# Performance work log

Hardware: AMD Instinct MI355X
Metric: run time of the kernel (lower is better)

## Reference

```python
import jax, jax.numpy as jnp
import numpy as np

B, T, C = 16, 4096, 64  # batch, seq_len, n_embd == head_size


def setup_inputs() -> dict:
    key = jax.random.key(0)
    k1, k2, k3, k4 = jax.random.split(key, 4)
    x = jax.random.normal(k1, (B, T, C), dtype=jnp.float32)
    Wq = jax.random.normal(k2, (C, C), dtype=jnp.float32) * (C ** -0.5)
    Wk = jax.random.normal(k3, (C, C), dtype=jnp.float32) * (C ** -0.5)
    Wv = jax.random.normal(k4, (C, C), dtype=jnp.float32) * (C ** -0.5)
    return {"x": x, "Wq": Wq, "Wk": Wk, "Wv": Wv}


def reference(x, Wq, Wk, Wv):
    # Single-head causal self-attention (dropout rate = 0.0 in source -> identity).
    q = jnp.einsum('btc,cd->btd', x, Wq)  # [B,T,D]
    k = jnp.einsum('btc,cd->btd', x, Wk)  # [B,T,D]
    v = jnp.einsum('btc,cd->btd', x, Wv)  # [B,T,D]
    scale = q.shape[-1] ** -0.5
    wei = jnp.einsum('btd,bsd->bts', q, k) * scale  # [B,T,T] scores
    causal = jnp.tril(jnp.ones((T, T), dtype=bool))  # [T,T]
    wei = jnp.where(causal[None, :, :], wei, jnp.finfo(wei.dtype).min)
    wei = jax.nn.softmax(wei, axis=-1)
    out = jnp.einsum('bts,bsd->btd', wei, v)  # [B,T,D]
    return out
```

## Files before the change

kernel.cpp:

```cpp
#include <hip/hip_runtime.h>
#include <hip/hip_bf16.h>
#include <math.h>

#define BATCH 16
#define SEQ 4096
#define HDIM 64

typedef __attribute__((ext_vector_type(8))) short bf16x8;
typedef __attribute__((ext_vector_type(4))) float f32x4;
typedef __attribute__((ext_vector_type(8))) unsigned short us8;

#define QSCALE 0.1803368801111601f

static __device__ __forceinline__ float exp2_fast(float x) {
#if __has_builtin(__builtin_amdgcn_exp2f)
    return __builtin_amdgcn_exp2f(x);
#else
    float r; asm("v_exp_f32 %0, %1" : "=v"(r) : "v"(x)); return r;
#endif
}

static __device__ __forceinline__ void load_lds16(const void* g, void* l) {
    __builtin_amdgcn_global_load_lds(
        (const __attribute__((address_space(1))) unsigned int*)g,
        (__attribute__((address_space(3))) unsigned int*)l,
        16, 0, 0);
}

static __device__ __forceinline__ unsigned short bf16bits(float f) {
    __hip_bfloat16 h = __float2bfloat16(f);
    return *(unsigned short*)&h;
}

__global__ __launch_bounds__(256)
void qkv_mfma_kernel(const float* __restrict__ x,
                     const float* __restrict__ Wq,
                     const float* __restrict__ Wk,
                     const float* __restrict__ Wv,
                     __hip_bfloat16* __restrict__ qb,
                     __hip_bfloat16* __restrict__ kb,
                     __hip_bfloat16* __restrict__ vt) {
    __shared__ __attribute__((aligned(16))) __hip_bfloat16 swt[3 * 64 * 64];
    __shared__ __attribute__((aligned(16))) __hip_bfloat16 sout[64][80];
    const int tid = threadIdx.x;
    const int wv = tid >> 6;
    const int lane = tid & 63;
    const int quad = lane >> 4;
    const int ml = lane & 15;
    const size_t row0 = (size_t)blockIdx.x * 64;
    const int batch = (int)(row0 >> 12);
    const int t0 = (int)(row0 & 4095);

    #pragma unroll
    for (int mat = 0; mat < 3; ++mat) {
        const float* W = (mat == 0) ? Wq : (mat == 1) ? Wk : Wv;
        const float sc = (mat == 0) ? QSCALE : 1.0f;
        const int n = tid & 63;
        #pragma unroll
        for (int i = 0; i < 16; ++i) {
            const int f = i * 256 + tid;
            const int k = f >> 6;
            swt[mat * 4096 + n * 64 + (((k >> 3) ^ (n & 7)) << 3) + (k & 7)] =
                __float2bfloat16(W[f] * sc);
        }
    }

    bf16x8 a0, a1;
    {
        const float4* xr = (const float4*)(x + (row0 + wv * 16 + ml) * HDIM);
        float4 lo = xr[quad * 2], hi = xr[quad * 2 + 1];
        float t8[8] = {lo.x, lo.y, lo.z, lo.w, hi.x, hi.y, hi.z, hi.w};
        #pragma unroll
        for (int j = 0; j < 8; ++j) a0[j] = (short)bf16bits(t8[j]);
        lo = xr[8 + quad * 2]; hi = xr[9 + quad * 2];
        float u8[8] = {lo.x, lo.y, lo.z, lo.w, hi.x, hi.y, hi.z, hi.w};
        #pragma unroll
        for (int j = 0; j < 8; ++j) a1[j] = (short)bf16bits(u8[j]);
    }
    __syncthreads();

    #pragma unroll
    for (int mat = 0; mat < 3; ++mat) {
        const __hip_bfloat16* wb = swt + mat * 4096;
        f32x4 acc[4];
        #pragma unroll
        for (int nt = 0; nt < 4; ++nt) {
            const int n = nt * 16 + ml;
            const int nx = n & 7;
            const bf16x8 bl = *(const bf16x8*)(wb + (size_t)n * 64 + (size_t)((quad) ^ nx) * 8);
            const bf16x8 bh = *(const bf16x8*)(wb + (size_t)n * 64 + (size_t)((quad + 4) ^ nx) * 8);
            acc[nt] = __builtin_amdgcn_mfma_f32_16x16x32_bf16(a0, bl, (f32x4){0.f,0.f,0.f,0.f}, 0, 0, 0);
            acc[nt] = __builtin_amdgcn_mfma_f32_16x16x32_bf16(a1, bh, acc[nt], 0, 0, 0);
        }

        if (mat < 2) {
            #pragma unroll
            for (int nt = 0; nt < 4; ++nt)
                #pragma unroll
                for (int r = 0; r < 4; ++r)
                    sout[wv * 16 + quad * 4 + r][nt * 16 + ml] = __float2bfloat16(acc[nt][r]);
        } else {
            #pragma unroll
            for (int nt = 0; nt < 4; ++nt)
                #pragma unroll
                for (int r = 0; r < 4; ++r)
                    sout[nt * 16 + ml][(wv >> 1) * 32 + quad * 8 + (wv & 1) * 4 + r] =
                        __float2bfloat16(acc[nt][r]);
        }
        __syncthreads();
        __hip_bfloat16* dst = (mat == 0) ? qb : (mat == 1) ? kb : vt;
        #pragma unroll
        for (int c2 = 0; c2 < 2; ++c2) {
            const int cc = c2 * 256 + tid;
            const int row = cc >> 3, g = cc & 7;
            us8 u = *(const us8*)&sout[row][g * 8];
            if (mat < 2)
                *(us8*)(dst + (row0 + row) * HDIM + g * 8) = u;
            else
                *(us8*)(dst + ((size_t)batch * HDIM + row) * SEQ + t0 + g * 8) = u;
        }
        __syncthreads();
    }
}

__global__ __launch_bounds__(256, 4)
void flash_mfma_kernel(const __hip_bfloat16* __restrict__ qb,
                       const __hip_bfloat16* __restrict__ kbuf,
                       const __hip_bfloat16* __restrict__ vt,
                       float* __restrict__ out) {
    __shared__ __attribute__((aligned(16))) __hip_bfloat16 sk[64 * 64];
    __shared__ __attribute__((aligned(16))) __hip_bfloat16 sv[64 * 64];
    __shared__ __attribute__((aligned(16))) float smerge[2][64][18];
    const int tid = threadIdx.x;
    const int wv = tid >> 6;
    const int lane = tid & 63;
    const int quad = lane >> 4;
    const int ml = lane & 15;
    const int mh = wv & 1;
    const int kh = wv >> 1;

    const int id = blockIdx.x;
    const int b = id & 15;
    const int t = id >> 4;
    const int hi2 = t >> 4, mid = t & 15;
    const int qt = (hi2 == 0) ? (63 - mid)
                 : (hi2 == 1) ? (32 + mid)
                 : (hi2 == 2) ? (31 - mid) : mid;
    const int qbw = qt * 64 + mh * 32;
    const size_t bb = (size_t)b * SEQ * HDIM;

    const __hip_bfloat16* Q = qb + bb;
    const __hip_bfloat16* K = kbuf + bb;
    const __hip_bfloat16* VT = vt + bb;

    bf16x8 bq[2][2];
    #pragma unroll
    for (int qi = 0; qi < 2; ++qi)
        #pragma unroll
        for (int h = 0; h < 2; ++h)
            bq[qi][h] = *(const bf16x8*)(Q + (size_t)(qbw + qi * 16 + ml) * HDIM + h * 32 + quad * 8);

    bf16x8 ones8;
    #pragma unroll
    for (int j = 0; j < 8; ++j) ones8[j] = (short)0x3F80;

    f32x4 acc[4][2];
    #pragma unroll
    for (int nt = 0; nt < 4; ++nt)
        #pragma unroll
        for (int qi = 0; qi < 2; ++qi) acc[nt][qi] = (f32x4){0.f, 0.f, 0.f, 0.f};
    f32x4 lacc[2] = {(f32x4){0.f,0.f,0.f,0.f}, (f32x4){0.f,0.f,0.f,0.f}};

    const int s0 = wv * 128 + lane;
    const int s1 = s0 + 64;
    const int r0row = s0 >> 3, r0ch = (s0 & 7) ^ (r0row & 7);
    const int r1row = s1 >> 3, r1ch = (s1 & 7) ^ (r1row & 7);
    __hip_bfloat16* ldsb0k = sk + (size_t)(wv * 128) * 8;
    __hip_bfloat16* ldsb1k = sk + (size_t)(wv * 128 + 64) * 8;
    __hip_bfloat16* ldsb0v = sv + (size_t)(wv * 128) * 8;
    __hip_bfloat16* ldsb1v = sv + (size_t)(wv * 128 + 64) * 8;

    const int rx = ml & 7;
    const int ntiles = qt + 1;
    for (int tile = 0; tile < ntiles; ++tile) {
        const int kb0 = tile * 64;
        __syncthreads();
        load_lds16(K + (size_t)(kb0 + r0row) * HDIM + r0ch * 8, ldsb0k);
        load_lds16(K + (size_t)(kb0 + r1row) * HDIM + r1ch * 8, ldsb1k);
        load_lds16(VT + (size_t)r0row * SEQ + kb0 + r0ch * 8, ldsb0v);
        load_lds16(VT + (size_t)r1row * SEQ + kb0 + r1ch * 8, ldsb1v);
        asm volatile("s_waitcnt vmcnt(0)" ::: "memory");
        __syncthreads();

        if (tile == qt && kh == 1 && mh == 0) continue;

        f32x4 st[2][2];
        #pragma unroll
        for (int kt = 0; kt < 2; ++kt) {
            const int row = kh * 32 + kt * 16 + ml;
            const int rb = row << 3, rxx = row & 7;
            const bf16x8 kl = *(const bf16x8*)(sk + (size_t)((rb | (quad ^ rxx)) * 8));
            const bf16x8 khi = *(const bf16x8*)(sk + (size_t)((rb | ((quad + 4) ^ rxx)) * 8));
            #pragma unroll
            for (int qi = 0; qi < 2; ++qi) {
                st[kt][qi] = __builtin_amdgcn_mfma_f32_16x16x32_bf16(kl, bq[qi][0], (f32x4){0.f,0.f,0.f,0.f}, 0, 0, 0);
                st[kt][qi] = __builtin_amdgcn_mfma_f32_16x16x32_bf16(khi, bq[qi][1], st[kt][qi], 0, 0, 0);
            }
        }

        const bool edge = (tile == qt);
        bf16x8 p8[2];
        #pragma unroll
        for (int qi = 0; qi < 2; ++qi) {
            const int q = qbw + qi * 16 + ml;
            #pragma unroll
            for (int half = 0; half < 2; ++half)
                #pragma unroll
                for (int r = 0; r < 4; ++r) {
                    const int key = kb0 + kh * 32 + half * 16 + quad * 4 + r;
                    float pv = exp2_fast(st[half][qi][r]);
                    if (edge && (key > q)) pv = 0.f;
                    p8[qi][half * 4 + r] = (short)bf16bits(pv);
                }
        }

        lacc[0] = __builtin_amdgcn_mfma_f32_16x16x32_bf16(ones8, p8[0], lacc[0], 0, 0, 0);
        lacc[1] = __builtin_amdgcn_mfma_f32_16x16x32_bf16(ones8, p8[1], lacc[1], 0, 0, 0);
        #pragma unroll
        for (int nt = 0; nt < 4; ++nt) {
            const int row = nt * 16 + ml;
            const int rb = row << 3, rxx = row & 7;
            const bf16x8 va = *(const bf16x8*)(sv + (size_t)((rb | ((kh * 4 + quad) ^ rxx)) * 8));
            acc[nt][0] = __builtin_amdgcn_mfma_f32_16x16x32_bf16(va, p8[0], acc[nt][0], 0, 0, 0);
            acc[nt][1] = __builtin_amdgcn_mfma_f32_16x16x32_bf16(va, p8[1], acc[nt][1], 0, 0, 0);
        }
    }

    #pragma unroll
    for (int qi = 0; qi < 2; ++qi) {
        __syncthreads();
        if (kh == 1) {
            float* mrow = smerge[mh][lane];
            #pragma unroll
            for (int nt = 0; nt < 4; ++nt)
                #pragma unroll
                for (int r = 0; r < 4; ++r) mrow[nt * 4 + r] = acc[nt][qi][r];
            mrow[16] = lacc[qi][0];
        }
        __syncthreads();
        if (kh == 0) {
            const float* mrow = smerge[mh][lane];
            const float inv = 1.0f / (lacc[qi][0] + mrow[16]);
            float* orow = out + bb + (size_t)(qbw + qi * 16 + ml) * HDIM;
            #pragma unroll
            for (int nt = 0; nt < 4; ++nt) {
                float4 o;
                o.x = (acc[nt][qi][0] + mrow[nt * 4 + 0]) * inv;
                o.y = (acc[nt][qi][1] + mrow[nt * 4 + 1]) * inv;
                o.z = (acc[nt][qi][2] + mrow[nt * 4 + 2]) * inv;
                o.w = (acc[nt][qi][3] + mrow[nt * 4 + 3]) * inv;
                *(float4*)(orow + nt * 16 + quad * 4) = o;
            }
        }
    }
}

extern "C" void kernel_launch(void* const* d_in, const int* in_sizes, int n_in,
                              void* d_out, int out_size, void* d_ws, size_t ws_size,
                              hipStream_t stream) {
    const float* x  = (const float*)d_in[0];
    const float* Wq = (const float*)d_in[1];
    const float* Wk = (const float*)d_in[2];
    const float* Wv = (const float*)d_in[3];
    float* outp = (float*)d_out;

    const size_t elems = (size_t)BATCH * SEQ * HDIM;
    __hip_bfloat16* qb = (__hip_bfloat16*)d_ws;
    __hip_bfloat16* kb = qb + elems;
    __hip_bfloat16* vt = kb + elems;

    qkv_mfma_kernel<<<dim3(BATCH * SEQ / 64), 256, 0, stream>>>(x, Wq, Wk, Wv, qb, kb, vt);
    flash_mfma_kernel<<<dim3(BATCH * SEQ / 64), 256, 0, stream>>>(qb, kb, vt, outp);
}
```

Measured before the change: 129.7 us.

## Load K/V fragments directly from global into registers, drop LDS staging

Each wave now reads its K and V^T MFMA fragments straight from global memory into registers, where before the whole block staged them through LDS with global_load_lds and two barriers per tile. K fragments for the next tile are prefetched while the current tile computes, and the wave that would skip the last causal tile now shortens its loop instead. This removes the per-tile __syncthreads and the LDS traffic. In exchange, K/V data is fetched redundantly by the waves that share it (more L2/global requests), the V loads are not prefetched, and register pressure rises.

```diff
diff --git a/kernel.cpp b/kernel.cpp
--- a/kernel.cpp
+++ b/kernel.cpp
@@ -18,13 +18,6 @@
 #else
     float r; asm("v_exp_f32 %0, %1" : "=v"(r) : "v"(x)); return r;
 #endif
-}
-
-static __device__ __forceinline__ void load_lds16(const void* g, void* l) {
-    __builtin_amdgcn_global_load_lds(
-        (const __attribute__((address_space(1))) unsigned int*)g,
-        (__attribute__((address_space(3))) unsigned int*)l,
-        16, 0, 0);
 }
 
 static __device__ __forceinline__ unsigned short bf16bits(float f) {
@@ -128,8 +121,6 @@
                        const __hip_bfloat16* __restrict__ kbuf,
                        const __hip_bfloat16* __restrict__ vt,
                        float* __restrict__ out) {
-    __shared__ __attribute__((aligned(16))) __hip_bfloat16 sk[64 * 64];
-    __shared__ __attribute__((aligned(16))) __hip_bfloat16 sv[64 * 64];
     __shared__ __attribute__((aligned(16))) float smerge[2][64][18];
     const int tid = threadIdx.x;
     const int wv = tid >> 6;
@@ -171,41 +162,41 @@
         for (int qi = 0; qi < 2; ++qi) acc[nt][qi] = (f32x4){0.f, 0.f, 0.f, 0.f};
     f32x4 lacc[2] = {(f32x4){0.f,0.f,0.f,0.f}, (f32x4){0.f,0.f,0.f,0.f}};
 
-    const int s0 = wv * 128 + lane;
-    const int s1 = s0 + 64;
-    const int r0row = s0 >> 3, r0ch = (s0 & 7) ^ (r0row & 7);
-    const int r1row = s1 >> 3, r1ch = (s1 & 7) ^ (r1row & 7);
-    __hip_bfloat16* ldsb0k = sk + (size_t)(wv * 128) * 8;
-    __hip_bfloat16* ldsb1k = sk + (size_t)(wv * 128 + 64) * 8;
-    __hip_bfloat16* ldsb0v = sv + (size_t)(wv * 128) * 8;
-    __hip_bfloat16* ldsb1v = sv + (size_t)(wv * 128 + 64) * 8;
-
-    const int rx = ml & 7;
-    const int ntiles = qt + 1;
+    const __hip_bfloat16* kp = K + (size_t)(kh * 32 + ml) * HDIM + quad * 8;
+    const __hip_bfloat16* vp = VT + (size_t)ml * SEQ + (kh * 4 + quad) * 8;
+
+    const int ntiles = qt + 1 - ((mh == 0 && kh == 1) ? 1 : 0);
+
+    bf16x8 kcur[2][2], knext[2][2], vf[4];
+    #pragma unroll
+    for (int kt = 0; kt < 2; ++kt)
+        #pragma unroll
+        for (int h = 0; h < 2; ++h)
+            kcur[kt][h] = *(const bf16x8*)(kp + kt * 16 * HDIM + h * 32);
+
     for (int tile = 0; tile < ntiles; ++tile) {
         const int kb0 = tile * 64;
-        __syncthreads();
-        load_lds16(K + (size_t)(kb0 + r0row) * HDIM + r0ch * 8, ldsb0k);
-        load_lds16(K + (size_t)(kb0 + r1row) * HDIM + r1ch * 8, ldsb1k);
-        load_lds16(VT + (size_t)r0row * SEQ + kb0 + r0ch * 8, ldsb0v);
-        load_lds16(VT + (size_t)r1row * SEQ + kb0 + r1ch * 8, ldsb1v);
-        asm volatile("s_waitcnt vmcnt(0)" ::: "memory");
-        __syncthreads();
-
-        if (tile == qt && kh == 1 && mh == 0) continue;
+
+        #pragma unroll
+        for (int nt = 0; nt < 4; ++nt)
+            vf[nt] = *(const bf16x8*)(vp + (size_t)nt * 16 * SEQ + kb0);
 
         f32x4 st[2][2];
         #pragma unroll
-        for (int kt = 0; kt < 2; ++kt) {
-            const int row = kh * 32 + kt * 16 + ml;
-            const int rb = row << 3, rxx = row & 7;
-            const bf16x8 kl = *(const bf16x8*)(sk + (size_t)((rb | (quad ^ rxx)) * 8));
-            const bf16x8 khi = *(const bf16x8*)(sk + (size_t)((rb | ((quad + 4) ^ rxx)) * 8));
+        for (int kt = 0; kt < 2; ++kt)
             #pragma unroll
             for (int qi = 0; qi < 2; ++qi) {
-                st[kt][qi] = __builtin_amdgcn_mfma_f32_16x16x32_bf16(kl, bq[qi][0], (f32x4){0.f,0.f,0.f,0.f}, 0, 0, 0);
-                st[kt][qi] = __builtin_amdgcn_mfma_f32_16x16x32_bf16(khi, bq[qi][1], st[kt][qi], 0, 0, 0);
+                st[kt][qi] = __builtin_amdgcn_mfma_f32_16x16x32_bf16(kcur[kt][0], bq[qi][0], (f32x4){0.f,0.f,0.f,0.f}, 0, 0, 0);
+                st[kt][qi] = __builtin_amdgcn_mfma_f32_16x16x32_bf16(kcur[kt][1], bq[qi][1], st[kt][qi], 0, 0, 0);
             }
+
+        if (tile + 1 < ntiles) {
+            const __hip_bfloat16* kn = kp + (size_t)(tile + 1) * 64 * HDIM;
+            #pragma unroll
+            for (int kt = 0; kt < 2; ++kt)
+                #pragma unroll
+                for (int h = 0; h < 2; ++h)
+                    knext[kt][h] = *(const bf16x8*)(kn + kt * 16 * HDIM + h * 32);
         }
 
         const bool edge = (tile == qt);
@@ -228,12 +219,15 @@
         lacc[1] = __builtin_amdgcn_mfma_f32_16x16x32_bf16(ones8, p8[1], lacc[1], 0, 0, 0);
         #pragma unroll
         for (int nt = 0; nt < 4; ++nt) {
-            const int row = nt * 16 + ml;
-            const int rb = row << 3, rxx = row & 7;
-            const bf16x8 va = *(const bf16x8*)(sv + (size_t)((rb | ((kh * 4 + quad) ^ rxx)) * 8));
-            acc[nt][0] = __builtin_amdgcn_mfma_f32_16x16x32_bf16(va, p8[0], acc[nt][0], 0, 0, 0);
-            acc[nt][1] = __builtin_amdgcn_mfma_f32_16x16x32_bf16(va, p8[1], acc[nt][1], 0, 0, 0);
-        }
+            acc[nt][0] = __builtin_amdgcn_mfma_f32_16x16x32_bf16(vf[nt], p8[0], acc[nt][0], 0, 0, 0);
+            acc[nt][1] = __builtin_amdgcn_mfma_f32_16x16x32_bf16(vf[nt], p8[1], acc[nt][1], 0, 0, 0);
+        }
+
+        #pragma unroll
+        for (int kt = 0; kt < 2; ++kt)
+            #pragma unroll
+            for (int h = 0; h < 2; ++h)
+                kcur[kt][h] = knext[kt][h];
     }
 
     #pragma unroll
```

Result: slower. 196.5 us (+51.6%).

## Double-buffer K/V tiles in LDS to overlap loads with MFMA compute

Applied to the files above, without the earlier changes.

Replaces the single K and V LDS buffers with one 32KB shared array that holds two K/V tile slots. The next tile is prefetched through global_load_lds into the alternate slot while the current tile is computed, so each iteration needs one barrier instead of two. The merge scratch space is aliased onto the same array after the loop. LDS use per block doubles, which may reduce how many blocks fit per CU, though it likely stays within the launch-bounds target of 4.

```diff
diff --git a/kernel.cpp b/kernel.cpp
--- a/kernel.cpp
+++ b/kernel.cpp
@@ -128,9 +128,8 @@
                        const __hip_bfloat16* __restrict__ kbuf,
                        const __hip_bfloat16* __restrict__ vt,
                        float* __restrict__ out) {
-    __shared__ __attribute__((aligned(16))) __hip_bfloat16 sk[64 * 64];
-    __shared__ __attribute__((aligned(16))) __hip_bfloat16 sv[64 * 64];
-    __shared__ __attribute__((aligned(16))) float smerge[2][64][18];
+    __shared__ __attribute__((aligned(16))) __hip_bfloat16 smem[16384];
+
     const int tid = threadIdx.x;
     const int wv = tid >> 6;
     const int lane = tid & 63;
@@ -175,67 +174,81 @@
     const int s1 = s0 + 64;
     const int r0row = s0 >> 3, r0ch = (s0 & 7) ^ (r0row & 7);
     const int r1row = s1 >> 3, r1ch = (s1 & 7) ^ (r1row & 7);
-    __hip_bfloat16* ldsb0k = sk + (size_t)(wv * 128) * 8;
-    __hip_bfloat16* ldsb1k = sk + (size_t)(wv * 128 + 64) * 8;
-    __hip_bfloat16* ldsb0v = sv + (size_t)(wv * 128) * 8;
-    __hip_bfloat16* ldsb1v = sv + (size_t)(wv * 128 + 64) * 8;
-
-    const int rx = ml & 7;
+    const int d0 = (wv * 128) * 8;
+    const int d1 = (wv * 128 + 64) * 8;
+
     const int ntiles = qt + 1;
+
+    load_lds16(K + (size_t)r0row * HDIM + r0ch * 8, smem + d0);
+    load_lds16(K + (size_t)r1row * HDIM + r1ch * 8, smem + d1);
+    load_lds16(VT + (size_t)r0row * SEQ + r0ch * 8, smem + 8192 + d0);
+    load_lds16(VT + (size_t)r1row * SEQ + r1ch * 8, smem + 8192 + d1);
+    asm volatile("s_waitcnt vmcnt(0)" ::: "memory");
+    __syncthreads();
+
     for (int tile = 0; tile < ntiles; ++tile) {
         const int kb0 = tile * 64;
-        __syncthreads();
-        load_lds16(K + (size_t)(kb0 + r0row) * HDIM + r0ch * 8, ldsb0k);
-        load_lds16(K + (size_t)(kb0 + r1row) * HDIM + r1ch * 8, ldsb1k);
-        load_lds16(VT + (size_t)r0row * SEQ + kb0 + r0ch * 8, ldsb0v);
-        load_lds16(VT + (size_t)r1row * SEQ + kb0 + r1ch * 8, ldsb1v);
+        const int sel = (tile & 1) * 4096;
+        const int nsel = 4096 - sel;
+        const __hip_bfloat16* sk = smem + sel;
+        const __hip_bfloat16* sv = smem + 8192 + sel;
+
+        if (tile + 1 < ntiles) {
+            const int nk = kb0 + 64;
+            load_lds16(K + (size_t)(nk + r0row) * HDIM + r0ch * 8, smem + nsel + d0);
+            load_lds16(K + (size_t)(nk + r1row) * HDIM + r1ch * 8, smem + nsel + d1);
+            load_lds16(VT + (size_t)r0row * SEQ + nk + r0ch * 8, smem + 8192 + nsel + d0);
+            load_lds16(VT + (size_t)r1row * SEQ + nk + r1ch * 8, smem + 8192 + nsel + d1);
+        }
+
+        if (!(tile == qt && kh == 1 && mh == 0)) {
+            f32x4 st[2][2];
+            #pragma unroll
+            for (int kt = 0; kt < 2; ++kt) {
+                const int row = kh * 32 + kt * 16 + ml;
+                const int rb = row << 3, rxx = row & 7;
+                const bf16x8 kl = *(const bf16x8*)(sk + (size_t)((rb | (quad ^ rxx)) * 8));
+                const bf16x8 khi = *(const bf16x8*)(sk + (size_t)((rb | ((quad + 4) ^ rxx)) * 8));
+                #pragma unroll
+                for (int qi = 0; qi < 2; ++qi) {
+                    st[kt][qi] = __builtin_amdgcn_mfma_f32_16x16x32_bf16(kl, bq[qi][0], (f32x4){0.f,0.f,0.f,0.f}, 0, 0, 0);
+                    st[kt][qi] = __builtin_amdgcn_mfma_f32_16x16x32_bf16(khi, bq[qi][1], st[kt][qi], 0, 0, 0);
+                }
+            }
+
+            const bool edge = (tile == qt);
+            bf16x8 p8[2];
+            #pragma unroll
+            for (int qi = 0; qi < 2; ++qi) {
+                const int q = qbw + qi * 16 + ml;
+                #pragma unroll
+                for (int half = 0; half < 2; ++half)
+                    #pragma unroll
+                    for (int r = 0; r < 4; ++r) {
+                        const int key = kb0 + kh * 32 + half * 16 + quad * 4 + r;
+                        float pv = exp2_fast(st[half][qi][r]);
+                        if (edge && (key > q)) pv = 0.f;
+                        p8[qi][half * 4 + r] = (short)bf16bits(pv);
+                    }
+            }
+
+            lacc[0] = __builtin_amdgcn_mfma_f32_16x16x32_bf16(ones8, p8[0], lacc[0], 0, 0, 0);
+            lacc[1] = __builtin_amdgcn_mfma_f32_16x16x32_bf16(ones8, p8[1], lacc[1], 0, 0, 0);
+            #pragma unroll
+            for (int nt = 0; nt < 4; ++nt) {
+                const int row = nt * 16 + ml;
+                const int rb = row << 3, rxx = row & 7;
+                const bf16x8 va = *(const bf16x8*)(sv + (size_t)((rb | ((kh * 4 + quad) ^ rxx)) * 8));
+                acc[nt][0] = __builtin_amdgcn_mfma_f32_16x16x32_bf16(va, p8[0], acc[nt][0], 0, 0, 0);
+                acc[nt][1] = __builtin_amdgcn_mfma_f32_16x16x32_bf16(va, p8[1], acc[nt][1], 0, 0, 0);
+            }
+        }
+
         asm volatile("s_waitcnt vmcnt(0)" ::: "memory");
         __syncthreads();
-
-        if (tile == qt && kh == 1 && mh == 0) continue;
-
-        f32x4 st[2][2];
-        #pragma unroll
-        for (int kt = 0; kt < 2; ++kt) {
-            const int row = kh * 32 + kt * 16 + ml;
-            const int rb = row << 3, rxx = row & 7;
-            const bf16x8 kl = *(const bf16x8*)(sk + (size_t)((rb | (quad ^ rxx)) * 8));
-            const bf16x8 khi = *(const bf16x8*)(sk + (size_t)((rb | ((quad + 4) ^ rxx)) * 8));
-            #pragma unroll
-            for (int qi = 0; qi < 2; ++qi) {
-                st[kt][qi] = __builtin_amdgcn_mfma_f32_16x16x32_bf16(kl, bq[qi][0], (f32x4){0.f,0.f,0.f,0.f}, 0, 0, 0);
-                st[kt][qi] = __builtin_amdgcn_mfma_f32_16x16x32_bf16(khi, bq[qi][1], st[kt][qi], 0, 0, 0);
-            }
-        }
-
-        const bool edge = (tile == qt);
-        bf16x8 p8[2];
-        #pragma unroll
-        for (int qi = 0; qi < 2; ++qi) {
-            const int q = qbw + qi * 16 + ml;
-            #pragma unroll
-            for (int half = 0; half < 2; ++half)
-                #pragma unroll
-                for (int r = 0; r < 4; ++r) {
-                    const int key = kb0 + kh * 32 + half * 16 + quad * 4 + r;
-                    float pv = exp2_fast(st[half][qi][r]);
-                    if (edge && (key > q)) pv = 0.f;
-                    p8[qi][half * 4 + r] = (short)bf16bits(pv);
-                }
-        }
-
-        lacc[0] = __builtin_amdgcn_mfma_f32_16x16x32_bf16(ones8, p8[0], lacc[0], 0, 0, 0);
-        lacc[1] = __builtin_amdgcn_mfma_f32_16x16x32_bf16(ones8, p8[1], lacc[1], 0, 0, 0);
-        #pragma unroll
-        for (int nt = 0; nt < 4; ++nt) {
-            const int row = nt * 16 + ml;
-            const int rb = row << 3, rxx = row & 7;
-            const bf16x8 va = *(const bf16x8*)(sv + (size_t)((rb | ((kh * 4 + quad) ^ rxx)) * 8));
-            acc[nt][0] = __builtin_amdgcn_mfma_f32_16x16x32_bf16(va, p8[0], acc[nt][0], 0, 0, 0);
-            acc[nt][1] = __builtin_amdgcn_mfma_f32_16x16x32_bf16(va, p8[1], acc[nt][1], 0, 0, 0);
-        }
-    }
-
+    }
+
+    float (*smerge)[64][18] = (float (*)[64][18])smem;
     #pragma unroll
     for (int qi = 0; qi < 2; ++qi) {
         __syncthreads();
```

After: 120.8 us. 6.8% less time.
